# Optimization experiments

Hardware: AMD Instinct MI355X
Metric: run time of the kernel (lower is better)

The kernel has to match this reference:

```python
import jax, jax.numpy as jnp
from jax import lax
import numpy as np

D_MODEL = 1024
D_STATE = 16
D_CONV = 4
EXPAND = 2
D_INNER = D_MODEL * EXPAND
EPS = 1e-5


def setup_inputs() -> dict:
    key = jax.random.key(0)
    ks = jax.random.split(key, 12)
    B, L = 2, 2048
    x = jax.random.normal(ks[0], (B, L, D_MODEL), jnp.float32)
    s = 0.02
    ln_g = jnp.ones((D_MODEL,), jnp.float32)
    ln_b = jnp.zeros((D_MODEL,), jnp.float32)
    W_in = jax.random.normal(ks[1], (D_MODEL, 2 * D_INNER), jnp.float32) * s
    conv_w = jax.random.normal(ks[2], (D_INNER, D_CONV), jnp.float32) * 0.2
    conv_b = jnp.zeros((D_INNER,), jnp.float32)
    W_xp = jax.random.normal(ks[3], (D_INNER, 2 * D_STATE + 1), jnp.float32) * s
    W_dt = jax.random.normal(ks[4], (1, D_INNER), jnp.float32) * s
    # dt bias init: inverse-softplus of dt ~ loguniform[dt_min, dt_max]
    dt = jnp.exp(jax.random.uniform(ks[5], (D_INNER,)) * (np.log(0.1) - np.log(0.001)) + np.log(0.001))
    b_dt = dt + jnp.log(-jnp.expm1(-dt))
    A_log = jnp.log(jnp.broadcast_to(jnp.arange(1, D_STATE + 1, dtype=jnp.float32)[None, :], (D_INNER, D_STATE)))
    D = jnp.ones((D_INNER,), jnp.float32)
    W_out = jax.random.normal(ks[6], (D_INNER, D_MODEL), jnp.float32) * s
    return {"x": x, "ln_g": ln_g, "ln_b": ln_b, "W_in": W_in, "conv_w": conv_w,
            "conv_b": conv_b, "W_xp": W_xp, "W_dt": W_dt, "b_dt": b_dt,
            "A_log": A_log, "D": D, "W_out": W_out}


def reference(x, ln_g, ln_b, W_in, conv_w, conv_b, W_xp, W_dt, b_dt, A_log, D, W_out):
    B, L, _ = x.shape
    residual = x
    # LayerNorm
    mu = jnp.mean(x, axis=-1, keepdims=True)
    var = jnp.mean(jnp.square(x - mu), axis=-1, keepdims=True)
    xn = (x - mu) * lax.rsqrt(var + EPS) * ln_g + ln_b
    # in_proj -> x, z
    xz = xn @ W_in                      # [B,L,2*di]
    xh, z = jnp.split(xz, 2, axis=-1)
    # depthwise causal conv1d (torch pads d_conv-1 both sides, truncates to L)
    xt = jnp.moveaxis(xh, 1, 2)         # [B,di,L]
    xp = jnp.pad(xt, ((0, 0), (0, 0), (D_CONV - 1, 0)))
    conv = conv_b[None, :, None]
    for k in range(D_CONV):             # tiny fixed-size loop
        conv = conv + conv_w[None, :, k, None] * xp[:, :, k:k + L]
    xc = jax.nn.silu(jnp.moveaxis(conv, 1, 2))  # [B,L,di]
    # SSM
    A = -jnp.exp(A_log)                 # [di,N]
    xpj = xc @ W_xp                     # [B,L,2N+1]
    Bm = xpj[..., :D_STATE]             # [B,L,N]
    Cm = xpj[..., D_STATE:2 * D_STATE]  # [B,L,N]
    dt = jax.nn.softplus(xpj[..., -1:] @ W_dt + b_dt)  # [B,L,di]
    dA = jnp.exp(dt[..., None] * A)                    # [B,L,di,N]
    dBx = (dt[..., None] * Bm[:, :, None, :]) * xc[..., None]  # [B,L,di,N]

    def step(h, inp):
        dAt, dBxt, Ct = inp
        h = dAt * h + dBxt
        y = jnp.einsum('bdn,bn->bd', h, Ct)
        return h, y

    h0 = jnp.zeros((B, D_INNER, D_STATE), x.dtype)
    _, ys = lax.scan(step, h0, (jnp.moveaxis(dA, 1, 0), jnp.moveaxis(dBx, 1, 0), jnp.moveaxis(Cm, 1, 0)))
    y = jnp.moveaxis(ys, 0, 1) + xc * D  # [B,L,di]
    out = (y * jax.nn.silu(z)) @ W_out
    return out + residual
```

## Files before the change

kernel.cpp:

```cpp
#include <hip/hip_runtime.h>
#include <math.h>

#define DM 1024
#define DS 16
#define DI 2048
#define LSEQ 2048
#define NBATCH 2
#define NTOK (NBATCH*LSEQ)
#define EPSV 1e-5f
#define NCHUNK 128
#define CLEN (LSEQ/NCHUNK)
#define XP_N 48
#define KSPLIT 8

#define LN_BLK   NTOK
#define WIN_BLK  (((2*DI)/64)*(DM/64))
#define WOUT_BLK ((DM/64)*(DI/64))
#define WXP_BLK  ((XP_N*DI)/256)

typedef __attribute__((ext_vector_type(8))) short bf16x8;
typedef __attribute__((ext_vector_type(4))) float f32x4;
typedef unsigned short u16;
typedef __attribute__((ext_vector_type(4))) unsigned short u16x4;
typedef __attribute__((ext_vector_type(8))) unsigned short u16x8;

__device__ __forceinline__ short f2bf(float f){
  union { float fv; unsigned u; } v; v.fv = f;
  unsigned u = v.u;
  return (short)((u + 0x7fffu + ((u >> 16) & 1u)) >> 16);
}
__device__ __forceinline__ u16 f2bfu(float f){ return (u16)f2bf(f); }
__device__ __forceinline__ float bf2f(u16 u){
  union { unsigned u; float f; } v; v.u = ((unsigned)u)<<16; return v.f;
}
__device__ __forceinline__ float sigmoidf_(float x){ return 1.f/(1.f+__expf(-x)); }
__device__ __forceinline__ float softplus_(float x){
  return (x > 20.f) ? x : log1pf(__expf(x));
}
__device__ __forceinline__ void gload16(const void* g, void* l){
  __builtin_amdgcn_global_load_lds(
      (const __attribute__((address_space(1))) void*)g,
      (__attribute__((address_space(3))) void*)l, 16, 0, 0);
}
__device__ __forceinline__ void powers16(float E1, float* dA){
  float E2=E1*E1, E4=E2*E2, E8=E4*E4, E3=E2*E1;
  dA[0]=E1;     dA[1]=E2;     dA[2]=E3;     dA[3]=E4;
  dA[4]=E4*E1;  dA[5]=E4*E2;  dA[6]=E4*E3;  dA[7]=E8;
  dA[8]=E8*E1;  dA[9]=E8*E2;  dA[10]=E8*E3; dA[11]=E8*E4;
  dA[12]=E8*dA[4]; dA[13]=E8*dA[5]; dA[14]=E8*dA[6]; dA[15]=E8*E8;
}

__global__ __launch_bounds__(256) void prep_kernel(const float* __restrict__ x,
    const float* __restrict__ ln_g, const float* __restrict__ ln_b,
    const float* __restrict__ W_in, const float* __restrict__ W_out,
    const float* __restrict__ W_xp,
    u16* __restrict__ xn, u16* __restrict__ winT, u16* __restrict__ woutT,
    u16* __restrict__ wt48)
{
  __shared__ float tile[64][65];
  int b = blockIdx.x;
  if (b < LN_BLK){
    int row = b;
    const float4* xin = (const float4*)(x + (size_t)row*DM);
    float4 v = xin[threadIdx.x];
    float s  = v.x+v.y+v.z+v.w;
    float s2 = v.x*v.x+v.y*v.y+v.z*v.z+v.w*v.w;
    #pragma unroll
    for (int m=1;m<64;m<<=1){ s += __shfl_xor(s,m,64); s2 += __shfl_xor(s2,m,64); }
    int w = threadIdx.x>>6;
    if ((threadIdx.x&63)==0){ tile[0][w]=s; tile[1][w]=s2; }
    __syncthreads();
    s  = tile[0][0]+tile[0][1]+tile[0][2]+tile[0][3];
    s2 = tile[1][0]+tile[1][1]+tile[1][2]+tile[1][3];
    float mu  = s*(1.f/DM);
    float var = s2*(1.f/DM) - mu*mu;
    float rs  = rsqrtf(var+EPSV);
    float4 gv = ((const float4*)ln_g)[threadIdx.x];
    float4 bv = ((const float4*)ln_b)[threadIdx.x];
    u16x4 o;
    o[0]=f2bfu((v.x-mu)*rs*gv.x+bv.x); o[1]=f2bfu((v.y-mu)*rs*gv.y+bv.y);
    o[2]=f2bfu((v.z-mu)*rs*gv.z+bv.z); o[3]=f2bfu((v.w-mu)*rs*gv.w+bv.w);
    *(u16x4*)(xn + (size_t)row*DM + threadIdx.x*4) = o;
    return;
  }
  b -= LN_BLK;
  if (b < WIN_BLK + WOUT_BLK){
    const float* W; u16* WT; int K, N, bx, by;
    if (b < WIN_BLK){ W = W_in; WT = winT; K = DM; N = 2*DI; bx = b & 63; by = b >> 6; }
    else { int bb = b - WIN_BLK; W = W_out; WT = woutT; K = DI; N = DM; bx = bb & 15; by = bb >> 4; }
    int n0 = bx*64, k0 = by*64;
    int tc = threadIdx.x & 63, tr = threadIdx.x >> 6;
    #pragma unroll
    for (int p=0;p<16;p++)
      tile[p*4+tr][tc] = W[(size_t)(k0 + p*4 + tr)*N + n0 + tc];
    __syncthreads();
    #pragma unroll
    for (int p=0;p<16;p++){
      int n = p*4 + tr;
      WT[(size_t)(n0+n)*K + k0 + tc] = f2bfu(tile[tc][n]);
    }
    return;
  }
  b -= WIN_BLK + WOUT_BLK;
  {
    int idx = b*256 + threadIdx.x;
    int j = idx >> 11;
    int k = idx & (DI-1);
    u16 v = 0;
    if (j < 33) v = f2bfu(W_xp[(size_t)k*33 + j]);
    wt48[idx] = v;
  }
}

__global__ __launch_bounds__(512) void gemm1_256(const u16* __restrict__ A,
    const u16* __restrict__ BT, u16* __restrict__ C)
{
  const int K = DM;
  const int NT = K >> 6;
  __shared__ __align__(16) u16 As[2*256*64];
  __shared__ __align__(16) u16 Bs[2*256*64];
  const int BUFO = 256*64;

  int bid = blockIdx.x;
  int xcd = bid & 7, idx = bid >> 3;
  int tx = (xcd&3)*4 + (idx>>3);
  int ty = (xcd>>2)*8 + (idx&7);

  int tid = threadIdx.x, w = tid>>6, lane = tid&63;
  int wm = w>>2, wn = w&3;
  int lr = lane&15, lk = lane>>4;
  int rg = lane>>3, c16 = lane&7;

  f32x4 acc[8][4] = {};

  const u16* aS[4]; const u16* bS[4];
  u16* aD[4]; u16* bD[4];
  #pragma unroll
  for (int q=0;q<4;q++){
    int rl = w*32 + q*8 + rg;
    aS[q] = A  + (size_t)(ty*256 + rl)*K + ((c16^rg)&7)*8;
    bS[q] = BT + (size_t)(tx*256 + rl)*K + ((c16^rg)&7)*8;
    aD[q] = &As[rl*64 + c16*8];
    bD[q] = &Bs[rl*64 + c16*8];
  }

  #pragma unroll
  for (int q=0;q<4;q++){ gload16(aS[q], aD[q]); gload16(bS[q], bD[q]); }

  int cur = 0;
  for (int t=0; t<NT; ++t){
    if (t+1 < NT){
      int k0 = (t+1) << 6;
      int off = (cur^1)*BUFO;
      #pragma unroll
      for (int q=0;q<4;q++){
        gload16(aS[q] + k0, aD[q] + off);
        gload16(bS[q] + k0, bD[q] + off);
      }
      asm volatile("s_waitcnt vmcnt(8)" ::: "memory");
    } else {
      asm volatile("s_waitcnt vmcnt(0)" ::: "memory");
    }
    __builtin_amdgcn_sched_barrier(0);
    __builtin_amdgcn_s_barrier();
    __builtin_amdgcn_sched_barrier(0);
    const u16* ab = &As[cur*BUFO];
    const u16* bb = &Bs[cur*BUFO];
    #pragma unroll
    for (int ph=0; ph<2; ++ph){
      bf16x8 af[8], bf[4];
      #pragma unroll
      for (int m=0;m<8;m++){
        int row = wm*128 + m*16 + lr;
        af[m] = *(const bf16x8*)&ab[row*64 + (((ph*4+lk)^(lr&7))&7)*8];
      }
      #pragma unroll
      for (int n=0;n<4;n++){
        int row = wn*64 + n*16 + lr;
        bf[n] = *(const bf16x8*)&bb[row*64 + (((ph*4+lk)^(lr&7))&7)*8];
      }
      __builtin_amdgcn_s_setprio(1);
      #pragma unroll
      for (int m=0;m<8;m++)
        #pragma unroll
        for (int n=0;n<4;n++)
          acc[m][n] = __builtin_amdgcn_mfma_f32_16x16x32_bf16(af[m], bf[n], acc[m][n], 0,0,0);
      __builtin_amdgcn_s_setprio(0);
    }
    asm volatile("s_waitcnt lgkmcnt(0)" ::: "memory");
    __builtin_amdgcn_sched_barrier(0);
    __builtin_amdgcn_s_barrier();
    cur ^= 1;
  }

  int grB = ty*256 + wm*128;
  int gcB = tx*256 + wn*64;
  #pragma unroll
  for (int m=0;m<8;m++){
    #pragma unroll
    for (int n=0;n<4;n++){
      int r0o = grB + m*16 + lk*4;
      int c  = gcB + n*16 + lr;
      #pragma unroll
      for (int r=0;r<4;r++)
        C[(size_t)(r0o+r)*(2*DI) + c] = f2bfu(acc[m][n][r]);
    }
  }
}

__global__ __launch_bounds__(256) void gemm2_kernel(const u16* __restrict__ A,
    const u16* __restrict__ BT, float* __restrict__ C, const float* __restrict__ R)
{
  const int K = DI;
  __shared__ __align__(16) u16 As[2*64*64];
  __shared__ __align__(16) u16 Bs[2*128*64];
  const int ABUF = 64*64, BBUF = 128*64;
  int bid = blockIdx.x;
  int xcd = bid & 7, idx = bid >> 3;
  int tx = idx >> 3;
  int ty = xcd*8 + (idx & 7);

  int tid = threadIdx.x, w = tid>>6, lane = tid&63;
  int lr = lane&15, lk = lane>>4;
  int rg = lane>>3, c16 = lane&7;
  f32x4 acc[4][2] = {};

  const u16* aS[2]; u16* aD[2];
  const u16* bS[4]; u16* bD[4];
  #pragma unroll
  for (int q=0;q<2;q++){
    int rl = w*16 + q*8 + rg;
    aS[q] = A + (size_t)(ty*64 + rl)*K + ((c16^rg)&7)*8;
    aD[q] = &As[rl*64 + c16*8];
  }
  #pragma unroll
  for (int q=0;q<4;q++){
    int rl = w*32 + q*8 + rg;
    bS[q] = BT + (size_t)(tx*128 + rl)*K + ((c16^rg)&7)*8;
    bD[q] = &Bs[rl*64 + c16*8];
  }

  int nt = K >> 6;
  #pragma unroll
  for (int q=0;q<2;q++) gload16(aS[q], aD[q]);
  #pragma unroll
  for (int q=0;q<4;q++) gload16(bS[q], bD[q]);

  int cur = 0;
  for (int t=0; t<nt; ++t){
    if (t+1 < nt){
      int k0 = (t+1) << 6;
      #pragma unroll
      for (int q=0;q<2;q++) gload16(aS[q] + k0, aD[q] + (cur^1)*ABUF);
      #pragma unroll
      for (int q=0;q<4;q++) gload16(bS[q] + k0, bD[q] + (cur^1)*BBUF);
      asm volatile("s_waitcnt vmcnt(6)" ::: "memory");
    } else {
      asm volatile("s_waitcnt vmcnt(0)" ::: "memory");
    }
    __builtin_amdgcn_sched_barrier(0);
    __builtin_amdgcn_s_barrier();
    __builtin_amdgcn_sched_barrier(0);
    const u16* ab = &As[cur*ABUF];
    const u16* bb = &Bs[cur*BBUF];
    #pragma unroll
    for (int kk=0;kk<2;kk++){
      bf16x8 af[4], bfv[2];
      #pragma unroll
      for (int i=0;i<4;i++){
        int row = i*16 + lr;
        af[i] = *(const bf16x8*)&ab[row*64 + (((kk*4+lk)^(lr&7))&7)*8];
      }
      #pragma unroll
      for (int j=0;j<2;j++){
        int row = w*32 + j*16 + lr;
        bfv[j] = *(const bf16x8*)&bb[row*64 + (((kk*4+lk)^(lr&7))&7)*8];
      }
      #pragma unroll
      for (int i=0;i<4;i++)
        #pragma unroll
        for (int j=0;j<2;j++)
          acc[i][j] = __builtin_amdgcn_mfma_f32_16x16x32_bf16(af[i], bfv[j], acc[i][j], 0,0,0);
    }
    asm volatile("s_waitcnt lgkmcnt(0)" ::: "memory");
    __builtin_amdgcn_sched_barrier(0);
    __builtin_amdgcn_s_barrier();
    cur ^= 1;
  }

  int grB = ty*64;
  int gcB = tx*128 + w*32;
  #pragma unroll
  for (int i=0;i<4;i++){
    #pragma unroll
    for (int j=0;j<2;j++){
      int r0 = grB + i*16 + lk*4;
      int c  = gcB + j*16 + lr;
      #pragma unroll
      for (int r=0;r<4;r++){
        float vv = acc[i][j][r] + R[(size_t)(r0+r)*DM + c];
        C[(size_t)(r0+r)*DM + c] = vv;
      }
    }
  }
}

__global__ __launch_bounds__(256) void conv_kernel(const u16* __restrict__ xz,
    const float* __restrict__ cw, const float* __restrict__ cb, u16* __restrict__ xc)
{
  int idx = blockIdx.x*256 + threadIdx.x;
  int d8 = (idx & (DI/8 - 1)) * 8;
  int t  = idx >> 8;
  int l  = t & (LSEQ-1);
  float4 cwv[8];
  #pragma unroll
  for (int j=0;j<8;j++) cwv[j] = *(const float4*)(cw + (size_t)(d8+j)*4);
  float acc[8];
  #pragma unroll
  for (int j=0;j<8;j++) acc[j] = cb[d8+j];
  #pragma unroll
  for (int k=0;k<4;k++){
    if (l + k >= 3){
      bf16x8 v = *(const bf16x8*)(xz + (size_t)(t+k-3)*(2*DI) + d8);
      #pragma unroll
      for (int j=0;j<8;j++){
        float wk = (k==0) ? cwv[j].x : (k==1) ? cwv[j].y : (k==2) ? cwv[j].z : cwv[j].w;
        acc[j] = fmaf(wk, bf2f((u16)v[j]), acc[j]);
      }
    }
  }
  bf16x8 o;
  #pragma unroll
  for (int j=0;j<8;j++){ float a = acc[j]; o[j] = f2bf(a * sigmoidf_(a)); }
  *(bf16x8*)(xc + (size_t)t*DI + d8) = o;
}

__global__ __launch_bounds__(256) void xpj_gemm(const u16* __restrict__ xc,
    const u16* __restrict__ WT48, float* __restrict__ Pbuf)
{
  __shared__ __align__(16) u16 As[4*64*64];
  __shared__ __align__(16) u16 Bs[4*48*64];
  int tid = threadIdx.x, w = tid>>6, lane = tid&63;
  int lr = lane&15, lk = lane>>4;
  f32x4 acc[3] = {};
  int mbase = blockIdx.x*64;
  int ky = blockIdx.y;
  int kgB = ky*256;

  #pragma unroll
  for (int s=0;s<4;s++){
    #pragma unroll
    for (int jj=0;jj<2;jj++){
      int ci = tid + jj*256;
      int rl = ci>>3, c16 = ci&7;
      gload16(xc + (size_t)(mbase+rl)*DI + kgB + s*64 + ((c16^(rl&7))&7)*8,
              &As[s*64*64 + rl*64 + c16*8]);
    }
  }
  if (tid < 192){
    #pragma unroll
    for (int s=0;s<4;s++){
      #pragma unroll
      for (int jj=0;jj<2;jj++){
        int ci = tid + jj*192;
        int rl = ci>>3, c16 = ci&7;
        gload16(WT48 + (size_t)rl*DI + kgB + s*64 + ((c16^(rl&7))&7)*8,
                &Bs[s*48*64 + rl*64 + c16*8]);
      }
    }
  }
  __syncthreads();

  #pragma unroll
  for (int s=0;s<4;s++){
    const u16* ab = &As[s*64*64];
    const u16* bb = &Bs[s*48*64];
    #pragma unroll
    for (int kk=0;kk<2;kk++){
      int arow = w*16 + lr;
      bf16x8 af = *(const bf16x8*)&ab[arow*64 + (((kk*4+lk)^(arow&7))&7)*8];
      #pragma unroll
      for (int j3=0;j3<3;j3++){
        int brow = j3*16 + lr;
        bf16x8 bfv = *(const bf16x8*)&bb[brow*64 + (((kk*4+lk)^(brow&7))&7)*8];
        acc[j3] = __builtin_amdgcn_mfma_f32_16x16x32_bf16(af, bfv, acc[j3], 0,0,0);
      }
    }
  }

  #pragma unroll
  for (int j3=0;j3<3;j3++){
    int col = j3*16 + lr;
    int r0 = w*16 + lk*4;
    #pragma unroll
    for (int r=0;r<4;r++){
      int t = mbase + r0 + r;
      Pbuf[((size_t)ky*NTOK + t)*XP_N + col] = acc[j3][r];
    }
  }
}

__global__ __launch_bounds__(256) void xpj_post(const float* __restrict__ Pbuf,
    const float* __restrict__ Wdt, const float* __restrict__ bdt,
    const u16* __restrict__ xcb, float* __restrict__ Bpl, float* __restrict__ Cpl,
    unsigned* __restrict__ dxb)
{
  __shared__ float s32sh;
  int t = blockIdx.x;
  int tid = threadIdx.x;
  if (tid < 33){
    float s = 0.f;
    #pragma unroll
    for (int ky=0;ky<KSPLIT;ky++) s += Pbuf[((size_t)ky*NTOK + t)*XP_N + tid];
    if (tid < 16)       Bpl[(size_t)t*16 + tid] = s;
    else if (tid < 32)  Cpl[(size_t)t*16 + (tid-16)] = s;
    else                s32sh = s;
  }
  __syncthreads();
  float s32 = s32sh;
  #pragma unroll
  for (int i=0;i<2;i++){
    int d4 = (tid + i*256)*4;
    float4 wv = *(const float4*)(Wdt + d4);
    float4 bv = *(const float4*)(bdt + d4);
    u16x4 xv = *(const u16x4*)(xcb + (size_t)t*DI + d4);
    uint4 o;
    o.x = (unsigned)(u16)f2bfu(softplus_(fmaf(s32, wv.x, bv.x))) | ((unsigned)xv[0]<<16);
    o.y = (unsigned)(u16)f2bfu(softplus_(fmaf(s32, wv.y, bv.y))) | ((unsigned)xv[1]<<16);
    o.z = (unsigned)(u16)f2bfu(softplus_(fmaf(s32, wv.z, bv.z))) | ((unsigned)xv[2]<<16);
    o.w = (unsigned)(u16)f2bfu(softplus_(fmaf(s32, wv.w, bv.w))) | ((unsigned)xv[3]<<16);
    *(uint4*)(dxb + (size_t)t*DI + d4) = o;
  }
}

__global__ __launch_bounds__(256) void scan_p1(const float* __restrict__ Bpl,
    const unsigned* __restrict__ dxb,
    u16* __restrict__ hend, float* __restrict__ Ssum)
{
  int bc = blockIdx.x >> 3;
  int d  = ((blockIdx.x & 7) << 8) + threadIdx.x;
  int c  = bc & (NCHUNK-1);
  int b  = bc >> 7;
  float h[16];
  #pragma unroll
  for (int n=0;n<16;n++) h[n] = 0.f;
  size_t t0 = (size_t)b*LSEQ + (size_t)c*CLEN;
  const unsigned* dxp = dxb + t0*DI + d;
  const f32x4* bp  = (const f32x4*)(Bpl + t0*16);
  float S = 0.f;
  #pragma unroll 4
  for (int l=0; l<CLEN; l++){
    unsigned pd = dxp[(size_t)l*DI];
    float dtv = bf2f((u16)(pd & 0xffffu));
    float xcv = bf2f((u16)(pd >> 16));
    float dxc = dtv*xcv;
    S += dtv;
    float E = __expf(-dtv);
    float dA[16];
    powers16(E, dA);
    f32x4 B0 = bp[l*4+0], B1 = bp[l*4+1], B2 = bp[l*4+2], B3 = bp[l*4+3];
    float Bv[16] = {B0[0],B0[1],B0[2],B0[3], B1[0],B1[1],B1[2],B1[3],
                    B2[0],B2[1],B2[2],B2[3], B3[0],B3[1],B3[2],B3[3]};
    #pragma unroll
    for (int n=0;n<16;n++)
      h[n] = fmaf(dA[n], h[n], dxc*Bv[n]);
  }
  size_t gid = (size_t)bc*DI + d;
  u16x8 p0, p1;
  #pragma unroll
  for (int n=0;n<8;n++){ p0[n] = f2bfu(h[n]); p1[n] = f2bfu(h[8+n]); }
  *(u16x8*)(hend + gid*16)     = p0;
  *(u16x8*)(hend + gid*16 + 8) = p1;
  Ssum[gid] = S;
}

__global__ __launch_bounds__(256) void scan_p2(u16* __restrict__ hend,
    const float* __restrict__ Ssum)
{
  int idx = blockIdx.x*256 + threadIdx.x;
  int n = idx & 15;
  int d = (idx >> 4) & (DI-1);
  int b = idx >> 15;
  float An = -(float)(n+1);
  float hs = 0.f;
  for (int cb=1; cb<NCHUNK; cb+=8){
    int nb = NCHUNK - cb; if (nb > 8) nb = 8;
    float he[8], Sv[8];
    #pragma unroll
    for (int i=0;i<8;i++){
      if (i<nb){
        size_t slot = ((size_t)(b*NCHUNK + cb+i-1)*DI + d);
        he[i] = bf2f(hend[slot*16 + n]);
        Sv[i] = Ssum[slot];
      }
    }
    #pragma unroll
    for (int i=0;i<8;i++){
      if (i<nb){
        size_t slot = ((size_t)(b*NCHUNK + cb+i-1)*DI + d);
        hs = fmaf(__expf(An*Sv[i]), hs, he[i]);
        hend[slot*16 + n] = f2bfu(hs);
      }
    }
  }
}

__global__ __launch_bounds__(256) void scan_p3(const float* __restrict__ Bpl,
    const float* __restrict__ Cpl, const unsigned* __restrict__ dxb,
    const u16* __restrict__ xz, const float* __restrict__ Dp,
    const u16* __restrict__ hend, u16* __restrict__ yg)
{
  int bc = blockIdx.x >> 3;
  int d  = ((blockIdx.x & 7) << 8) + threadIdx.x;
  int c  = bc & (NCHUNK-1);
  int b  = bc >> 7;
  size_t gid = (size_t)bc*DI + d;
  float h[16];
  #pragma unroll
  for (int n=0;n<16;n++) h[n] = 0.f;
  if (c > 0){
    u16x8 p0 = *(const u16x8*)(hend + (gid - DI)*16);
    u16x8 p1 = *(const u16x8*)(hend + (gid - DI)*16 + 8);
    #pragma unroll
    for (int n=0;n<8;n++){ h[n] = bf2f(p0[n]); h[8+n] = bf2f(p1[n]); }
  }
  float Dd = Dp[d];
  size_t t0 = (size_t)b*LSEQ + (size_t)c*CLEN;
  const unsigned* dxp = dxb + t0*DI + d;
  const u16* zp  = xz  + t0*(2*DI) + DI + d;
  const f32x4* bp  = (const f32x4*)(Bpl + t0*16);
  const f32x4* cp  = (const f32x4*)(Cpl + t0*16);
  u16* yp          = yg  + t0*DI + d;
  #pragma unroll 4
  for (int l=0; l<CLEN; l++){
    unsigned pd = dxp[(size_t)l*DI];
    float dtv = bf2f((u16)(pd & 0xffffu));
    float xcv = bf2f((u16)(pd >> 16));
    float dxc = dtv*xcv;
    float E = __expf(-dtv);
    float dA[16];
    powers16(E, dA);
    f32x4 B0 = bp[l*4+0], B1 = bp[l*4+1], B2 = bp[l*4+2], B3 = bp[l*4+3];
    f32x4 C0 = cp[l*4+0], C1 = cp[l*4+1], C2 = cp[l*4+2], C3 = cp[l*4+3];
    float Bv[16] = {B0[0],B0[1],B0[2],B0[3], B1[0],B1[1],B1[2],B1[3],
                    B2[0],B2[1],B2[2],B2[3], B3[0],B3[1],B3[2],B3[3]};
    float Cv[16] = {C0[0],C0[1],C0[2],C0[3], C1[0],C1[1],C1[2],C1[3],
                    C2[0],C2[1],C2[2],C2[3], C3[0],C3[1],C3[2],C3[3]};
    float a0=0.f, a1=0.f, a2=0.f, a3=0.f;
    #pragma unroll
    for (int n=0;n<16;n+=4){
      h[n+0] = fmaf(dA[n+0], h[n+0], dxc*Bv[n+0]);
      h[n+1] = fmaf(dA[n+1], h[n+1], dxc*Bv[n+1]);
      h[n+2] = fmaf(dA[n+2], h[n+2], dxc*Bv[n+2]);
      h[n+3] = fmaf(dA[n+3], h[n+3], dxc*Bv[n+3]);
      a0 = fmaf(h[n+0], Cv[n+0], a0);
      a1 = fmaf(h[n+1], Cv[n+1], a1);
      a2 = fmaf(h[n+2], Cv[n+2], a2);
      a3 = fmaf(h[n+3], Cv[n+3], a3);
    }
    float acc = (a0+a1) + (a2+a3);
    float zv = bf2f(zp[(size_t)l*2*DI]);
    yp[(size_t)l*DI] = f2bfu(fmaf(xcv, Dd, acc) * (zv * sigmoidf_(zv)));
  }
}

extern "C" void kernel_launch(void* const* d_in, const int* in_sizes, int n_in,
                              void* d_out, int out_size, void* d_ws, size_t ws_size,
                              hipStream_t stream)
{
  (void)in_sizes; (void)n_in; (void)out_size; (void)ws_size;
  const float* x      = (const float*)d_in[0];
  const float* ln_g   = (const float*)d_in[1];
  const float* ln_b   = (const float*)d_in[2];
  const float* W_in   = (const float*)d_in[3];
  const float* conv_w = (const float*)d_in[4];
  const float* conv_b = (const float*)d_in[5];
  const float* W_xp   = (const float*)d_in[6];
  const float* W_dt   = (const float*)d_in[7];
  const float* b_dt   = (const float*)d_in[8];
  const float* A_log  = (const float*)d_in[9];  (void)A_log;
  const float* Dp     = (const float*)d_in[10];
  const float* W_out  = (const float*)d_in[11];
  float* out = (float*)d_out;

  u16* xnb   = (u16*)d_ws;
  u16* ygb   = xnb + (size_t)NTOK*DM;
  u16* winT  = ygb + (size_t)NTOK*DI;
  u16* woutT = winT + (size_t)2*DI*DM;
  u16* xzb   = woutT + (size_t)DM*DI;
  u16* xcb   = xzb + (size_t)NTOK*2*DI;
  unsigned* dxb = (unsigned*)(xcb + (size_t)NTOK*DI);
  u16* wt48  = (u16*)(dxb + (size_t)NTOK*DI);
  float* xf  = (float*)(wt48 + (size_t)XP_N*DI);
  float* Bpl  = xf;
  float* Cpl  = Bpl + (size_t)NTOK*16;
  float* Ssum = Cpl + (size_t)NTOK*16;
  float* Pbuf = Ssum + (size_t)NBATCH*NCHUNK*DI;
  u16* hend  = (u16*)(Pbuf + (size_t)KSPLIT*NTOK*XP_N);

  hipLaunchKernelGGL(prep_kernel, dim3(LN_BLK+WIN_BLK+WOUT_BLK+WXP_BLK), dim3(256), 0, stream,
                     x, ln_g, ln_b, W_in, W_out, W_xp, xnb, winT, woutT, wt48);
  hipLaunchKernelGGL(gemm1_256, dim3(256), dim3(512), 0, stream,
                     xnb, winT, xzb);
  hipLaunchKernelGGL(conv_kernel, dim3((NTOK*DI/8)/256), dim3(256), 0, stream,
                     xzb, conv_w, conv_b, xcb);
  hipLaunchKernelGGL(xpj_gemm, dim3(NTOK/64, KSPLIT), dim3(256), 0, stream,
                     xcb, wt48, Pbuf);
  hipLaunchKernelGGL(xpj_post, dim3(NTOK), dim3(256), 0, stream,
                     Pbuf, W_dt, b_dt, xcb, Bpl, Cpl, dxb);
  hipLaunchKernelGGL(scan_p1, dim3(NBATCH*NCHUNK*DI/256), dim3(256), 0, stream,
                     Bpl, dxb, hend, Ssum);
  hipLaunchKernelGGL(scan_p2, dim3(NBATCH*DI*16/256), dim3(256), 0, stream,
                     hend, Ssum);
  hipLaunchKernelGGL(scan_p3, dim3(NBATCH*NCHUNK*DI/256), dim3(256), 0, stream,
                     Bpl, Cpl, dxb, xzb, Dp, hend, ygb);
  hipLaunchKernelGGL(gemm2_kernel, dim3(512), dim3(256), 0, stream,
                     ygb, woutT, out, x);
}
```

Baseline: 213.5 us.

## Retile output projection GEMM to 128x128 blocks with 512 threads and K=128 stages

Rewrites the output-projection GEMM to use 128x128 output tiles per 512-thread block (8 waves in a 2x4 grid), K-steps of 128 with a 16-way XOR LDS swizzle, and s_setprio around the MFMA bursts. Larger tiles raise operand reuse from LDS and halve global loads per FLOP. In exchange the grid shrinks to 256 blocks (about one per CU), LDS use grows to 128KB per block, and fewer blocks are left to hide latency and tail effects.

```diff
diff --git a/kernel.cpp b/kernel.cpp
--- a/kernel.cpp
+++ b/kernel.cpp
@@ -208,79 +208,83 @@
   }
 }
 
-__global__ __launch_bounds__(256) void gemm2_kernel(const u16* __restrict__ A,
+__global__ __launch_bounds__(512) void gemm2_128(const u16* __restrict__ A,
     const u16* __restrict__ BT, float* __restrict__ C, const float* __restrict__ R)
 {
   const int K = DI;
-  __shared__ __align__(16) u16 As[2*64*64];
-  __shared__ __align__(16) u16 Bs[2*128*64];
-  const int ABUF = 64*64, BBUF = 128*64;
+  const int NT = K >> 7;
+  __shared__ __align__(16) u16 As[2*128*128];
+  __shared__ __align__(16) u16 Bs[2*128*128];
+  const int BUFO = 128*128;
+
   int bid = blockIdx.x;
   int xcd = bid & 7, idx = bid >> 3;
-  int tx = idx >> 3;
-  int ty = xcd*8 + (idx & 7);
+  int ty = xcd*4 + (idx&3);
+  int tx = idx>>2;
 
   int tid = threadIdx.x, w = tid>>6, lane = tid&63;
+  int wm = w>>2, wn = w&3;
   int lr = lane&15, lk = lane>>4;
-  int rg = lane>>3, c16 = lane&7;
+
   f32x4 acc[4][2] = {};
 
-  const u16* aS[2]; u16* aD[2];
-  const u16* bS[4]; u16* bD[4];
-  #pragma unroll
-  for (int q=0;q<2;q++){
-    int rl = w*16 + q*8 + rg;
-    aS[q] = A + (size_t)(ty*64 + rl)*K + ((c16^rg)&7)*8;
-    aD[q] = &As[rl*64 + c16*8];
-  }
+  int rq0 = tid>>4;
+  int c16 = tid&15;
+  int swz = rq0 & 15;
+  int cgl = c16 ^ swz;
+  const u16* aS[4]; const u16* bS[4];
+  u16* aD[4]; u16* bD[4];
   #pragma unroll
   for (int q=0;q<4;q++){
-    int rl = w*32 + q*8 + rg;
-    bS[q] = BT + (size_t)(tx*128 + rl)*K + ((c16^rg)&7)*8;
-    bD[q] = &Bs[rl*64 + c16*8];
-  }
-
-  int nt = K >> 6;
-  #pragma unroll
-  for (int q=0;q<2;q++) gload16(aS[q], aD[q]);
-  #pragma unroll
-  for (int q=0;q<4;q++) gload16(bS[q], bD[q]);
+    int rl = q*32 + rq0;
+    aS[q] = A  + (size_t)(ty*128 + rl)*K + cgl*8;
+    bS[q] = BT + (size_t)(tx*128 + rl)*K + cgl*8;
+    aD[q] = &As[rl*128 + c16*8];
+    bD[q] = &Bs[rl*128 + c16*8];
+  }
+
+  #pragma unroll
+  for (int q=0;q<4;q++){ gload16(aS[q], aD[q]); gload16(bS[q], bD[q]); }
 
   int cur = 0;
-  for (int t=0; t<nt; ++t){
-    if (t+1 < nt){
-      int k0 = (t+1) << 6;
-      #pragma unroll
-      for (int q=0;q<2;q++) gload16(aS[q] + k0, aD[q] + (cur^1)*ABUF);
-      #pragma unroll
-      for (int q=0;q<4;q++) gload16(bS[q] + k0, bD[q] + (cur^1)*BBUF);
-      asm volatile("s_waitcnt vmcnt(6)" ::: "memory");
+  for (int t=0; t<NT; ++t){
+    if (t+1 < NT){
+      int k0 = (t+1) << 7;
+      int off = (cur^1)*BUFO;
+      #pragma unroll
+      for (int q=0;q<4;q++){
+        gload16(aS[q] + k0, aD[q] + off);
+        gload16(bS[q] + k0, bD[q] + off);
+      }
+      asm volatile("s_waitcnt vmcnt(8)" ::: "memory");
     } else {
       asm volatile("s_waitcnt vmcnt(0)" ::: "memory");
     }
     __builtin_amdgcn_sched_barrier(0);
     __builtin_amdgcn_s_barrier();
     __builtin_amdgcn_sched_barrier(0);
-    const u16* ab = &As[cur*ABUF];
-    const u16* bb = &Bs[cur*BBUF];
-    #pragma unroll
-    for (int kk=0;kk<2;kk++){
-      bf16x8 af[4], bfv[2];
-      #pragma unroll
-      for (int i=0;i<4;i++){
-        int row = i*16 + lr;
-        af[i] = *(const bf16x8*)&ab[row*64 + (((kk*4+lk)^(lr&7))&7)*8];
-      }
-      #pragma unroll
-      for (int j=0;j<2;j++){
-        int row = w*32 + j*16 + lr;
-        bfv[j] = *(const bf16x8*)&bb[row*64 + (((kk*4+lk)^(lr&7))&7)*8];
-      }
-      #pragma unroll
-      for (int i=0;i<4;i++)
+    const u16* ab = &As[cur*BUFO];
+    const u16* bb = &Bs[cur*BUFO];
+    #pragma unroll
+    for (int kk=0; kk<4; ++kk){
+      bf16x8 af[4], bf[2];
+      #pragma unroll
+      for (int m=0;m<4;m++){
+        int row = wm*64 + m*16 + lr;
+        af[m] = *(const bf16x8*)&ab[row*128 + (((kk*4+lk)^(row&15))&15)*8];
+      }
+      #pragma unroll
+      for (int n=0;n<2;n++){
+        int row = wn*32 + n*16 + lr;
+        bf[n] = *(const bf16x8*)&bb[row*128 + (((kk*4+lk)^(row&15))&15)*8];
+      }
+      __builtin_amdgcn_s_setprio(1);
+      #pragma unroll
+      for (int m=0;m<4;m++)
         #pragma unroll
-        for (int j=0;j<2;j++)
-          acc[i][j] = __builtin_amdgcn_mfma_f32_16x16x32_bf16(af[i], bfv[j], acc[i][j], 0,0,0);
+        for (int n=0;n<2;n++)
+          acc[m][n] = __builtin_amdgcn_mfma_f32_16x16x32_bf16(af[m], bf[n], acc[m][n], 0,0,0);
+      __builtin_amdgcn_s_setprio(0);
     }
     asm volatile("s_waitcnt lgkmcnt(0)" ::: "memory");
     __builtin_amdgcn_sched_barrier(0);
@@ -288,17 +292,17 @@
     cur ^= 1;
   }
 
-  int grB = ty*64;
-  int gcB = tx*128 + w*32;
-  #pragma unroll
-  for (int i=0;i<4;i++){
-    #pragma unroll
-    for (int j=0;j<2;j++){
-      int r0 = grB + i*16 + lk*4;
-      int c  = gcB + j*16 + lr;
+  int grB = ty*128 + wm*64;
+  int gcB = tx*128 + wn*32;
+  #pragma unroll
+  for (int m=0;m<4;m++){
+    #pragma unroll
+    for (int n=0;n<2;n++){
+      int r0 = grB + m*16 + lk*4;
+      int c  = gcB + n*16 + lr;
       #pragma unroll
       for (int r=0;r<4;r++){
-        float vv = acc[i][j][r] + R[(size_t)(r0+r)*DM + c];
+        float vv = acc[m][n][r] + R[(size_t)(r0+r)*DM + c];
         C[(size_t)(r0+r)*DM + c] = vv;
       }
     }
@@ -614,6 +618,6 @@
                      hend, Ssum);
   hipLaunchKernelGGL(scan_p3, dim3(NBATCH*NCHUNK*DI/256), dim3(256), 0, stream,
                      Bpl, Cpl, dxb, xzb, Dp, hend, ygb);
-  hipLaunchKernelGGL(gemm2_kernel, dim3(512), dim3(256), 0, stream,
+  hipLaunchKernelGGL(gemm2_128, dim3(256), dim3(512), 0, stream,
                      ygb, woutT, out, x);
 }
```

Measured after the change: 210.8 us, median of 2. Within noise of the previous version (-1.3%).
